# Performance work log

Hardware: AMD Instinct MI355X
Metric: run time of the kernel (lower is better)

Reference implementation:

```python
import jax, jax.numpy as jnp
import numpy as np

H = 1024

def setup_inputs() -> dict:
    key = jax.random.key(0)
    ks = jax.random.split(key, 9)
    s = 1.0 / np.sqrt(H)
    x = jax.random.normal(ks[0], (4, 2048, H), dtype=jnp.float32)
    Wq = jax.random.uniform(ks[1], (H, H), jnp.float32, -s, s)
    bq = jax.random.uniform(ks[2], (H,), jnp.float32, -s, s)
    Wk = jax.random.uniform(ks[3], (H, H), jnp.float32, -s, s)
    bk = jax.random.uniform(ks[4], (H,), jnp.float32, -s, s)
    Wv = jax.random.uniform(ks[5], (H, H), jnp.float32, -s, s)
    bv = jax.random.uniform(ks[6], (H,), jnp.float32, -s, s)
    Wo = jax.random.uniform(ks[7], (H, H), jnp.float32, -s, s)
    bo = jax.random.uniform(ks[8], (H,), jnp.float32, -s, s)
    return {"x": x, "Wq": Wq, "bq": bq, "Wk": Wk, "bk": bk,
            "Wv": Wv, "bv": bv, "Wo": Wo, "bo": bo}

def reference(x, Wq, bq, Wk, bk, Wv, bv, Wo, bo):
    # Linear uses y = x @ W.T + b (torch convention: W is [out, in])
    q = jnp.einsum('bsd,ed->bse', x, Wq) + bq
    k = jnp.einsum('bsd,ed->bse', x, Wk) + bk
    v = jnp.einsum('bsd,ed->bse', x, Wv) + bv
    scale = q.shape[-1] ** 0.5
    attn = jnp.einsum('bqe,bke->bqk', q, k) / scale  # [B,S,S]
    attn = jax.nn.softmax(attn, axis=-1)
    out = jnp.einsum('bqk,bke->bqe', attn, v)
    return jnp.einsum('bse,oe->bso', out, Wo) + bo
```

## Files before the change

### kernel.cpp

```cpp
#include <hip/hip_runtime.h>

typedef short  short4v __attribute__((ext_vector_type(4)));
typedef short  short8v __attribute__((ext_vector_type(8)));
typedef __bf16 bf16x8  __attribute__((ext_vector_type(8)));
typedef float  f32x4   __attribute__((ext_vector_type(4)));
typedef float  float4v __attribute__((ext_vector_type(4)));

__device__ __forceinline__ short f2bf(float f) {
  unsigned u = __builtin_bit_cast(unsigned, f);
  u += 0x7fffu + ((u >> 16) & 1u);
  return (short)(u >> 16);
}
__device__ __forceinline__ float bf2f(short h) {
  unsigned u = ((unsigned)(unsigned short)h) << 16;
  return __builtin_bit_cast(float, u);
}
__device__ __forceinline__ bf16x8 ld8(const short* p) {
  return __builtin_bit_cast(bf16x8, *reinterpret_cast<const short8v*>(p));
}

__constant__ const float kExpScale = 0.04508422f;

__global__ __launch_bounds__(256) void k_inprep(
    const float* __restrict__ x, short* __restrict__ xb,
    const float* __restrict__ i0, const float* __restrict__ i1,
    const float* __restrict__ i2, const float* __restrict__ i3,
    short* __restrict__ o0, short* __restrict__ o1,
    short* __restrict__ o2, short* __restrict__ o3) {
  const int bid = blockIdx.x;
  const int tid = threadIdx.x;
  if (bid < 2048) {
    const int i = bid * 256 + tid;
#pragma unroll
    for (int j = 0; j < 4; ++j) {
      const long g = (long)i + (long)j * 524288;
      float4v v = *reinterpret_cast<const float4v*>(x + g * 4);
      short4v o;
      o[0] = f2bf(v[0]); o[1] = f2bf(v[1]); o[2] = f2bf(v[2]); o[3] = f2bf(v[3]);
      *reinterpret_cast<short4v*>(xb + g * 4) = o;
    }
    return;
  }
  const int w = bid - 2048;
  const int z = w >> 7;
  const int rem = w & 127;
  const int c0 = (rem & 15) << 6;
  const int r0 = (rem >> 4) << 7;
  const float* in = z == 0 ? i0 : z == 1 ? i1 : z == 2 ? i2 : i3;
  short* out = z == 0 ? o0 : z == 1 ? o1 : z == 2 ? o2 : o3;
  const float sc = (z == 1) ? kExpScale : 1.0f;
  if (z == 3) {
#pragma unroll
    for (int j = 0; j < 8; ++j) {
      int idx = j * 256 + tid;
      int r = idx >> 4, c4 = (idx & 15) << 2;
      float4v v = *reinterpret_cast<const float4v*>(in + (long)(r0 + r) * 1024 + c0 + c4);
      short4v o;
      o[0] = f2bf(v[0]); o[1] = f2bf(v[1]); o[2] = f2bf(v[2]); o[3] = f2bf(v[3]);
      *reinterpret_cast<short4v*>(out + (long)(r0 + r) * 1024 + c0 + c4) = o;
    }
    return;
  }
  __shared__ float tile[128][65];
#pragma unroll
  for (int j = 0; j < 8; ++j) {
    int idx = j * 256 + tid;
    int r = idx >> 4, c4 = (idx & 15) << 2;
    float4v v = *reinterpret_cast<const float4v*>(in + (long)(r0 + r) * 1024 + c0 + c4);
    tile[r][c4 + 0] = v[0] * sc; tile[r][c4 + 1] = v[1] * sc;
    tile[r][c4 + 2] = v[2] * sc; tile[r][c4 + 3] = v[3] * sc;
  }
  __syncthreads();
#pragma unroll
  for (int j = 0; j < 8; ++j) {
    int idx = j * 256 + tid;
    int rO = idx >> 5, g4 = (idx & 31) << 2;
    short4v o;
    o[0] = f2bf(tile[g4 + 0][rO]); o[1] = f2bf(tile[g4 + 1][rO]);
    o[2] = f2bf(tile[g4 + 2][rO]); o[3] = f2bf(tile[g4 + 3][rO]);
    *reinterpret_cast<short4v*>(out + (long)(c0 + rO) * 1024 + r0 + g4) = o;
  }
}

__device__ __forceinline__ void gemm_loop(const short* __restrict__ Ab,
    const short* __restrict__ Bb, int K, int lda, int ldb, int bm, int bn,
    f32x4 (&acc)[4][4]) {
  __shared__ __align__(16) short lsA[128 * 64];
  __shared__ __align__(16) short lsB[128 * 64];
  const int tid = threadIdx.x;
  const int lane = tid & 63, wid = tid >> 6;
  const int wr = wid >> 1, wc = wid & 1;
  const int fr = lane & 15, fq = lane >> 4;
  for (int kt = 0; kt < K; kt += 64) {
    __syncthreads();
#pragma unroll
    for (int c = 0; c < 4; ++c) {
      const int idx = c * 256 + tid;
      const int row = idx >> 3, colh = (idx & 7) << 3;
      const short* ga = Ab + (long)(bm + row) * lda + kt + colh;
      const short* gb = Bb + (long)(bn + row) * ldb + kt + colh;
      __builtin_amdgcn_global_load_lds(
          (const __attribute__((address_space(1))) void*)ga,
          (__attribute__((address_space(3))) void*)&lsA[idx * 8], 16, 0, 0);
      __builtin_amdgcn_global_load_lds(
          (const __attribute__((address_space(1))) void*)gb,
          (__attribute__((address_space(3))) void*)&lsB[idx * 8], 16, 0, 0);
    }
    __syncthreads();
#pragma unroll
    for (int ks = 0; ks < 64; ks += 32) {
      bf16x8 a[4], b[4];
#pragma unroll
      for (int m = 0; m < 4; ++m)
        a[m] = ld8(&lsA[(wr * 64 + m * 16 + fr) * 64 + ks + fq * 8]);
#pragma unroll
      for (int n = 0; n < 4; ++n)
        b[n] = ld8(&lsB[(wc * 64 + n * 16 + fr) * 64 + ks + fq * 8]);
#pragma unroll
      for (int m = 0; m < 4; ++m)
#pragma unroll
        for (int n = 0; n < 4; ++n)
          acc[m][n] = __builtin_amdgcn_mfma_f32_16x16x32_bf16(a[m], b[n], acc[m][n], 0, 0, 0);
    }
  }
}

__device__ __forceinline__ void gemm_loop_w(const short* __restrict__ Ab,
    const short* __restrict__ Bb, int K, int lda, int ldb, int bm, int bn,
    f32x4 (&acc)[4][4]) {
  __shared__ __align__(16) short lsA[128 * 64];
  __shared__ __align__(16) short lsB[256 * 64];
  const int tid = threadIdx.x;
  const int lane = tid & 63, wid = tid >> 6;
  const int wr = wid >> 2, wc = wid & 3;
  const int fr = lane & 15, fq = lane >> 4;
  for (int kt = 0; kt < K; kt += 64) {
    __syncthreads();
#pragma unroll
    for (int c = 0; c < 2; ++c) {
      const int idx = c * 512 + tid;
      const int row = idx >> 3, colh = (idx & 7) << 3;
      __builtin_amdgcn_global_load_lds(
          (const __attribute__((address_space(1))) void*)
              (Ab + (long)(bm + row) * lda + kt + colh),
          (__attribute__((address_space(3))) void*)&lsA[idx * 8], 16, 0, 0);
    }
#pragma unroll
    for (int c = 0; c < 4; ++c) {
      const int idx = c * 512 + tid;
      const int row = idx >> 3, colh = (idx & 7) << 3;
      __builtin_amdgcn_global_load_lds(
          (const __attribute__((address_space(1))) void*)
              (Bb + (long)(bn + row) * ldb + kt + colh),
          (__attribute__((address_space(3))) void*)&lsB[idx * 8], 16, 0, 0);
    }
    __syncthreads();
#pragma unroll
    for (int ks = 0; ks < 64; ks += 32) {
      bf16x8 a[4], b[4];
#pragma unroll
      for (int m = 0; m < 4; ++m)
        a[m] = ld8(&lsA[(wr * 64 + m * 16 + fr) * 64 + ks + fq * 8]);
#pragma unroll
      for (int n = 0; n < 4; ++n)
        b[n] = ld8(&lsB[(wc * 64 + n * 16 + fr) * 64 + ks + fq * 8]);
#pragma unroll
      for (int m = 0; m < 4; ++m)
#pragma unroll
        for (int n = 0; n < 4; ++n)
          acc[m][n] = __builtin_amdgcn_mfma_f32_16x16x32_bf16(a[m], b[n], acc[m][n], 0, 0, 0);
    }
  }
}

__global__ __launch_bounds__(256, 3) void k_prep2(
    const short* __restrict__ wkT, const short* __restrict__ wqT,
    const short* __restrict__ wob, const short* __restrict__ wvT,
    const float* __restrict__ bq, const float* __restrict__ Wo,
    const float* __restrict__ bv,
    short* __restrict__ mt, short* __restrict__ wv2,
    float* __restrict__ bvec, float* __restrict__ bvp) {
  const int tid = threadIdx.x;
  const int lane = tid & 63, wid = tid >> 6;
  if (blockIdx.z == 2) {
    const int r0 = (blockIdx.y * 8 + blockIdx.x) * 16;
#pragma unroll
    for (int rr = 0; rr < 4; ++rr) {
      const int row = r0 + wid * 4 + rr;
      {
        const short* xr = wkT + (long)row * 1024 + lane * 16;
        short8v a0 = *reinterpret_cast<const short8v*>(xr);
        short8v a1 = *reinterpret_cast<const short8v*>(xr + 8);
        float s = 0.f;
#pragma unroll
        for (int j = 0; j < 8; ++j) s += bf2f(a0[j]) * bq[lane * 16 + j];
#pragma unroll
        for (int j = 0; j < 8; ++j) s += bf2f(a1[j]) * bq[lane * 16 + 8 + j];
#pragma unroll
        for (int off = 32; off; off >>= 1) s += __shfl_xor(s, off);
        if (lane == 0) bvec[row] = s * kExpScale;
      }
      {
        float s = 0.f;
#pragma unroll
        for (int j = 0; j < 16; ++j)
          s += Wo[(long)row * 1024 + j * 64 + lane] * bv[j * 64 + lane];
#pragma unroll
        for (int off = 32; off; off >>= 1) s += __shfl_xor(s, off);
        if (lane == 0) bvp[row] = s;
      }
    }
    return;
  }
  const short* A = blockIdx.z == 0 ? wkT : wob;
  const short* B = blockIdx.z == 0 ? wqT : wvT;
  short* C = blockIdx.z == 0 ? mt : wv2;
  const int bm = blockIdx.x * 128, bn = blockIdx.y * 128;
  f32x4 acc[4][4] = {};
  gemm_loop(A, B, 1024, 1024, 1024, bm, bn, acc);
  const int wr = wid >> 1, wc = wid & 1;
  const int fr = lane & 15, fq = lane >> 4;
#pragma unroll
  for (int n = 0; n < 4; ++n) {
    const int col = bn + wc * 64 + n * 16 + fr;
#pragma unroll
    for (int m = 0; m < 4; ++m) {
      const int row0 = bm + wr * 64 + m * 16 + fq * 4;
#pragma unroll
      for (int i = 0; i < 4; ++i)
        C[(long)(row0 + i) * 1024 + col] = f2bf(acc[m][n][i]);
    }
  }
}

__global__ __launch_bounds__(256, 3) void k_gemmTV(
    const short* __restrict__ xb, const short* __restrict__ mt,
    const short* __restrict__ wv2, const float* __restrict__ bvp,
    const float* __restrict__ bvec, short* __restrict__ T,
    short* __restrict__ vTp, float* __restrict__ w8) {
  const int tid = threadIdx.x;
  const int lane = tid & 63, wid = tid >> 6;
  if (blockIdx.z == 2) {
    const int rbase = (blockIdx.x * 8 + blockIdx.y) * 16;
#pragma unroll
    for (int rr = 0; rr < 4; ++rr) {
      const int row = rbase + wid * 4 + rr;
      const short* xr = xb + (long)row * 1024 + lane * 16;
      short8v a0 = *reinterpret_cast<const short8v*>(xr);
      short8v a1 = *reinterpret_cast<const short8v*>(xr + 8);
      float s = 0.f;
#pragma unroll
      for (int j = 0; j < 8; ++j) s += bf2f(a0[j]) * bvec[lane * 16 + j];
#pragma unroll
      for (int j = 0; j < 8; ++j) s += bf2f(a1[j]) * bvec[lane * 16 + 8 + j];
#pragma unroll
      for (int off = 32; off; off >>= 1) s += __shfl_xor(s, off);
      if (lane == 0) w8[row] = s;
    }
    return;
  }
  const short *A, *B; const float* bias; short* C; int ldC, bm, bn;
  if (blockIdx.z == 0) {
    A = xb; B = mt; bias = nullptr; C = T; ldC = 1024;
    bm = blockIdx.x * 128; bn = blockIdx.y * 128;
  } else {
    A = wv2; B = xb; bias = bvp; C = vTp; ldC = 8192;
    bm = blockIdx.y * 128; bn = blockIdx.x * 128;
  }
  f32x4 acc[4][4] = {};
  gemm_loop(A, B, 1024, 1024, 1024, bm, bn, acc);
  const int wr = wid >> 1, wc = wid & 1;
  const int fr = lane & 15, fq = lane >> 4;
#pragma unroll
  for (int n = 0; n < 4; ++n) {
    const int col = bn + wc * 64 + n * 16 + fr;
#pragma unroll
    for (int m = 0; m < 4; ++m) {
      const int row0 = bm + wr * 64 + m * 16 + fq * 4;
#pragma unroll
      for (int i = 0; i < 4; ++i) {
        const float bvr = bias ? bias[row0 + i] : 0.f;
        C[(long)(row0 + i) * ldC + col] = f2bf(acc[m][n][i] + bvr);
      }
    }
  }
}

__global__ __launch_bounds__(512, 2) void k_scores(
    const short* __restrict__ A, const short* __restrict__ B,
    const float* __restrict__ b0p, float* __restrict__ b1p,
    short* __restrict__ C0,
    int K, long sA, long sB, long sC, int ldC) {
  const int tid = threadIdx.x;
  const int lane = tid & 63, wid = tid >> 6;
  const int wr = wid >> 2, wc = wid & 3;
  const int fr = lane & 15, fq = lane >> 4;
  const int bm = blockIdx.x * 128, bn = blockIdx.y * 256;
  const int bz = blockIdx.z;

  f32x4 acc[4][4] = {};
  gemm_loop_w(A + (long)bz * sA, B + (long)bz * sB, K, K, K, bm, bn, acc);

  short* O = C0 + (long)bz * sC;
  float wv[4];
#pragma unroll
  for (int n = 0; n < 4; ++n)
    wv[n] = b0p[(long)bz * 2048 + bn + wc * 64 + n * 16 + fr];
#pragma unroll
  for (int m = 0; m < 4; ++m) {
#pragma unroll
    for (int i = 0; i < 4; ++i) {
      const int row = bm + wr * 64 + m * 16 + fq * 4 + i;
      float rs = 0.f;
#pragma unroll
      for (int n = 0; n < 4; ++n) {
        float e = exp2f(acc[m][n][i] + wv[n]);
        O[(long)row * ldC + bn + wc * 64 + n * 16 + fr] = f2bf(e);
        rs += e;
      }
      rs += __shfl_xor(rs, 1); rs += __shfl_xor(rs, 2);
      rs += __shfl_xor(rs, 4); rs += __shfl_xor(rs, 8);
      if (fr == 0)
        b1p[((long)bz * 2048 + row) * 32 + blockIdx.y * 4 + wc] = rs;
    }
  }
}

__global__ __launch_bounds__(256, 3) void k_pv(
    const short* __restrict__ A, const short* __restrict__ B,
    const float* __restrict__ b0p, float* __restrict__ b1p,
    float* __restrict__ C0,
    int K, int lda, int ldb, long sA, long sB, long sC, int ldC) {
  __shared__ float invL[128];
  const int tid = threadIdx.x;
  const int lane = tid & 63, wid = tid >> 6;
  const int wr = wid >> 1, wc = wid & 1;
  const int fr = lane & 15, fq = lane >> 4;
  const int bm = blockIdx.x * 128, bn = blockIdx.y * 128;
  const int bz = blockIdx.z;

  {
    const int row = tid >> 1, half = tid & 1;
    const float* pr = b1p + ((long)bz * 2048 + bm + row) * 32 + half * 16;
    float s = 0.f;
#pragma unroll
    for (int j = 0; j < 4; ++j) {
      float4v v = *reinterpret_cast<const float4v*>(pr + j * 4);
      s += v[0] + v[1] + v[2] + v[3];
    }
    s += __shfl_xor(s, 1);
    if (half == 0) invL[row] = 1.0f / s;
  }

  f32x4 acc[4][4] = {};
  gemm_loop(A + (long)bz * sA, B + (long)bz * sB, K, lda, ldb, bm, bn, acc);

#pragma unroll
  for (int n = 0; n < 4; ++n) {
    const int coll = wc * 64 + n * 16 + fr;
#pragma unroll
    for (int m = 0; m < 4; ++m) {
      const int rl0 = wr * 64 + m * 16 + fq * 4;
#pragma unroll
      for (int i = 0; i < 4; ++i) {
        const long row = bm + rl0 + i, col = bn + coll;
        float* O = C0 + (long)bz * sC;
        O[row * ldC + col] = acc[m][n][i] * invL[rl0 + i] + b0p[col];
      }
    }
  }
}

extern "C" void kernel_launch(void* const* d_in, const int* in_sizes, int n_in,
                              void* d_out, int out_size, void* d_ws, size_t ws_size,
                              hipStream_t stream) {
  const float* x  = (const float*)d_in[0];
  const float* Wq = (const float*)d_in[1];
  const float* bq = (const float*)d_in[2];
  const float* Wk = (const float*)d_in[3];
  const float* Wv = (const float*)d_in[5];
  const float* bv = (const float*)d_in[6];
  const float* Wo = (const float*)d_in[7];
  const float* bo = (const float*)d_in[8];

  char* ws = (char*)d_ws;
  short* xb   = (short*)ws; ws += 8192L * 1024 * 2;
  short* wkT  = (short*)ws; ws += 1024L * 1024 * 2;
  short* wob  = (short*)ws; ws += 1024L * 1024 * 2;
  short* wqT  = (short*)ws; ws += 1024L * 1024 * 2;
  short* wvT  = (short*)ws; ws += 1024L * 1024 * 2;
  short* mt   = (short*)ws; ws += 1024L * 1024 * 2;
  short* wv2  = (short*)ws; ws += 1024L * 1024 * 2;
  short* T    = (short*)ws; ws += 8192L * 1024 * 2;
  short* vTp  = (short*)ws; ws += 1024L * 8192 * 2;
  short* Sc   = (short*)ws; ws += 4L * 2048 * 2048 * 2;
  float* psum = (float*)ws; ws += 4L * 2048 * 32 * 4;
  float* w8   = (float*)ws; ws += 8192L * 4;
  float* bvec = (float*)ws; ws += 1024L * 4;
  float* bvp  = (float*)ws; ws += 1024L * 4;

  dim3 b256(256), b512(512);
  k_inprep<<<2560, b256, 0, stream>>>(
      x, xb, Wk, Wq, Wv, Wo, wkT, wqT, wvT, wob);
  k_prep2<<<dim3(8, 8, 3), b256, 0, stream>>>(
      wkT, wqT, wob, wvT, bq, Wo, bv, mt, wv2, bvec, bvp);
  k_gemmTV<<<dim3(64, 8, 3), b256, 0, stream>>>(
      xb, mt, wv2, bvp, bvec, T, vTp, w8);
  k_scores<<<dim3(16, 8, 4), b512, 0, stream>>>(
      T, xb, w8, psum, Sc,
      1024, 2048L * 1024, 2048L * 1024, 2048L * 2048, 2048);
  k_pv<<<dim3(16, 8, 4), b256, 0, stream>>>(
      Sc, vTp, bo, psum, (float*)d_out,
      2048, 2048, 8192, 2048L * 2048, 2048, 2048L * 1024, 1024);
}
```

Measured before the change: 187.3 us.

## Fuse T and V projection GEMMs into one kernel sharing the x tile

The two separate GEMM launches (T = x·M and vT = Wv2·xᵀ) become a single kernel in which each block loads one x tile into LDS and reuses it as the A operand for T and the B operand for V. This halves the global loads of x across the two GEMMs. The w8 row-dot blocks are remapped into an extra grid column. In exchange each block holds two accumulator sets and three LDS buffers, and the new loop is single-buffered rather than using the shared gemm_loop. That raises register and LDS pressure and may lower occupancy.

```diff
diff --git a/kernel.cpp b/kernel.cpp
--- a/kernel.cpp
+++ b/kernel.cpp
@@ -233,18 +233,18 @@
   }
 }
 
-__global__ __launch_bounds__(256, 3) void k_gemmTV(
+__global__ __launch_bounds__(256, 3) void k_tvf(
     const short* __restrict__ xb, const short* __restrict__ mt,
     const short* __restrict__ wv2, const float* __restrict__ bvp,
     const float* __restrict__ bvec, short* __restrict__ T,
     short* __restrict__ vTp, float* __restrict__ w8) {
   const int tid = threadIdx.x;
   const int lane = tid & 63, wid = tid >> 6;
-  if (blockIdx.z == 2) {
-    const int rbase = (blockIdx.x * 8 + blockIdx.y) * 16;
-#pragma unroll
-    for (int rr = 0; rr < 4; ++rr) {
-      const int row = rbase + wid * 4 + rr;
+  if (blockIdx.y == 8) {
+    const int rbase = blockIdx.x * 128 + wid * 32;
+#pragma unroll 4
+    for (int rr = 0; rr < 32; ++rr) {
+      const int row = rbase + rr;
       const short* xr = xb + (long)row * 1024 + lane * 16;
       short8v a0 = *reinterpret_cast<const short8v*>(xr);
       short8v a1 = *reinterpret_cast<const short8v*>(xr + 8);
@@ -259,28 +259,73 @@
     }
     return;
   }
-  const short *A, *B; const float* bias; short* C; int ldC, bm, bn;
-  if (blockIdx.z == 0) {
-    A = xb; B = mt; bias = nullptr; C = T; ldC = 1024;
-    bm = blockIdx.x * 128; bn = blockIdx.y * 128;
-  } else {
-    A = wv2; B = xb; bias = bvp; C = vTp; ldC = 8192;
-    bm = blockIdx.y * 128; bn = blockIdx.x * 128;
-  }
-  f32x4 acc[4][4] = {};
-  gemm_loop(A, B, 1024, 1024, 1024, bm, bn, acc);
+  __shared__ __align__(16) short lsX[8192];
+  __shared__ __align__(16) short lsM[8192];
+  __shared__ __align__(16) short lsW[8192];
   const int wr = wid >> 1, wc = wid & 1;
   const int fr = lane & 15, fq = lane >> 4;
+  const int bm = blockIdx.x * 128;
+  const int jb = blockIdx.y * 128;
+  const short* Xb = xb + (long)bm * 1024;
+  const short* Mb = mt + (long)jb * 1024;
+  const short* Wb = wv2 + (long)jb * 1024;
+
+  f32x4 accT[4][4] = {}, accV[4][4] = {};
+
+  for (int kt = 0; kt < 1024; kt += 64) {
+    __syncthreads();
+#pragma unroll
+    for (int c = 0; c < 4; ++c) {
+      const int idx = c * 256 + tid;
+      const int row = idx >> 3, colh = (idx & 7) << 3;
+      const long off = (long)row * 1024 + kt + colh;
+      __builtin_amdgcn_global_load_lds(
+          (const __attribute__((address_space(1))) void*)(Xb + off),
+          (__attribute__((address_space(3))) void*)&lsX[idx * 8], 16, 0, 0);
+      __builtin_amdgcn_global_load_lds(
+          (const __attribute__((address_space(1))) void*)(Mb + off),
+          (__attribute__((address_space(3))) void*)&lsM[idx * 8], 16, 0, 0);
+      __builtin_amdgcn_global_load_lds(
+          (const __attribute__((address_space(1))) void*)(Wb + off),
+          (__attribute__((address_space(3))) void*)&lsW[idx * 8], 16, 0, 0);
+    }
+    __syncthreads();
+#pragma unroll
+    for (int ks = 0; ks < 64; ks += 32) {
+      bf16x8 xa[4], xn[4], mb[4], wa[4];
+#pragma unroll
+      for (int m = 0; m < 4; ++m)
+        xa[m] = ld8(&lsX[(wr * 64 + m * 16 + fr) * 64 + ks + fq * 8]);
+#pragma unroll
+      for (int n = 0; n < 4; ++n)
+        xn[n] = ld8(&lsX[(wc * 64 + n * 16 + fr) * 64 + ks + fq * 8]);
+#pragma unroll
+      for (int n = 0; n < 4; ++n)
+        mb[n] = ld8(&lsM[(wc * 64 + n * 16 + fr) * 64 + ks + fq * 8]);
+#pragma unroll
+      for (int m = 0; m < 4; ++m)
+        wa[m] = ld8(&lsW[(wr * 64 + m * 16 + fr) * 64 + ks + fq * 8]);
+#pragma unroll
+      for (int m = 0; m < 4; ++m)
+#pragma unroll
+        for (int n = 0; n < 4; ++n) {
+          accT[m][n] = __builtin_amdgcn_mfma_f32_16x16x32_bf16(xa[m], mb[n], accT[m][n], 0, 0, 0);
+          accV[m][n] = __builtin_amdgcn_mfma_f32_16x16x32_bf16(wa[m], xn[n], accV[m][n], 0, 0, 0);
+        }
+    }
+  }
+
 #pragma unroll
   for (int n = 0; n < 4; ++n) {
-    const int col = bn + wc * 64 + n * 16 + fr;
+    const int coln = wc * 64 + n * 16 + fr;
 #pragma unroll
     for (int m = 0; m < 4; ++m) {
-      const int row0 = bm + wr * 64 + m * 16 + fq * 4;
+      const int rowm = wr * 64 + m * 16 + fq * 4;
 #pragma unroll
       for (int i = 0; i < 4; ++i) {
-        const float bvr = bias ? bias[row0 + i] : 0.f;
-        C[(long)(row0 + i) * ldC + col] = f2bf(acc[m][n][i] + bvr);
+        T[(long)(bm + rowm + i) * 1024 + jb + coln] = f2bf(accT[m][n][i]);
+        vTp[(long)(jb + rowm + i) * 8192 + bm + coln] =
+            f2bf(accV[m][n][i] + bvp[jb + rowm + i]);
       }
     }
   }
@@ -404,7 +449,7 @@
       x, xb, Wk, Wq, Wv, Wo, wkT, wqT, wvT, wob);
   k_prep2<<<dim3(8, 8, 3), b256, 0, stream>>>(
       wkT, wqT, wob, wvT, bq, Wo, bv, mt, wv2, bvec, bvp);
-  k_gemmTV<<<dim3(64, 8, 3), b256, 0, stream>>>(
+  k_tvf<<<dim3(64, 9, 1), b256, 0, stream>>>(
       xb, mt, wv2, bvp, bvec, T, vTp, w8);
   k_scores<<<dim3(16, 8, 4), b512, 0, stream>>>(
       T, xb, w8, psum, Sc,
```

Result: slower. 198.5 us (+6.0%).
